# Optimization experiments

Measured on AMD Instinct MI355X. Metric: run time of the kernel, lower is better.

Reference implementation:

```python
import jax, jax.numpy as jnp
import numpy as np

N_NODES = 50000
N_EDGES = 800000
IN_DIM = 128
HID = 64
OUT_DIM = 128
N_GRAPHS = 256


def setup_inputs() -> dict:
    key = jax.random.key(0)
    ks = jax.random.split(key, 8)
    x = jax.random.normal(ks[0], (N_NODES, IN_DIM), dtype=jnp.float32)
    edge_index = jax.random.randint(ks[1], (2, N_EDGES), 0, N_NODES, dtype=jnp.int64)
    batch = jnp.sort(jax.random.randint(ks[2], (N_NODES,), 0, N_GRAPHS, dtype=jnp.int64))
    # Glorot-ish init for GCN weights, zero bias (PyG default bias=True)
    W1 = jax.random.normal(ks[3], (IN_DIM, HID), dtype=jnp.float32) / np.sqrt(IN_DIM)
    b1 = jnp.zeros((HID,), dtype=jnp.float32)
    W2 = jax.random.normal(ks[4], (HID, HID), dtype=jnp.float32) / np.sqrt(HID)
    b2 = jnp.zeros((HID,), dtype=jnp.float32)
    W3 = jax.random.normal(ks[5], (HID, OUT_DIM), dtype=jnp.float32) / np.sqrt(HID)
    b3 = jnp.zeros((OUT_DIM,), dtype=jnp.float32)
    return {"x": x, "edge_index": edge_index, "batch": batch, "num_graphs": N_GRAPHS,
            "W1": W1, "b1": b1, "W2": W2, "b2": b2, "W3": W3, "b3": b3}


def _gcn_norm(edge_index, n_nodes):
    # PyG GCNConv default: add self-loops, symmetric D^{-1/2}(A+I)D^{-1/2} norm.
    loops = jnp.arange(n_nodes, dtype=edge_index.dtype)
    src = jnp.concatenate([edge_index[0], loops])  # [E + N]
    dst = jnp.concatenate([edge_index[1], loops])
    deg = jax.ops.segment_sum(jnp.ones_like(dst, dtype=jnp.float32), dst,
                              num_segments=n_nodes)
    dinv = jnp.where(deg > 0, jax.lax.rsqrt(jnp.maximum(deg, 1.0)), 0.0)
    norm = dinv[src] * dinv[dst]  # [E + N]
    return src, dst, norm


def _gcn_conv(x, W, b, src, dst, norm, n_nodes):
    h = x @ W                                  # [N, F_out] dense GEMM
    msg = h[src] * norm[:, None]               # gather + scale  [E+N, F_out]
    agg = jax.ops.segment_sum(msg, dst, num_segments=n_nodes)
    return agg + b


def reference(x, edge_index, batch, num_graphs, W1, b1, W2, b2, W3, b3):
    n_nodes = x.shape[0]
    src, dst, norm = _gcn_norm(edge_index, n_nodes)
    h = jax.nn.gelu(_gcn_conv(x, W1, b1, src, dst, norm, n_nodes))
    h = jax.nn.gelu(_gcn_conv(h, W2, b2, src, dst, norm, n_nodes))
    h = _gcn_conv(h, W3, b3, src, dst, norm, n_nodes)
    # global_mean_pool over batch segment ids
    sums = jax.ops.segment_sum(h, batch, num_segments=num_graphs)
    counts = jax.ops.segment_sum(jnp.ones((n_nodes,), dtype=h.dtype), batch,
                                 num_segments=num_graphs)
    return sums / jnp.maximum(counts, 1.0)[:, None]
```

## Files before the change

### kernel.cpp

```cpp
#include <hip/hip_runtime.h>
#include <hip/hip_fp16.h>
#include <math.h>

#define N_NODES   50000
#define N_EDGES   800000
#define IN_DIM    128
#define HID       64
#define OUT_DIM   128
#define N_GRAPHS  256
#define MAX_DEG   64
#define PARTS     8
#define PSIZE     (N_NODES / PARTS)
#define EPB       4096
#define AGG_NPB   32

typedef _Float16 half8 __attribute__((ext_vector_type(8)));
typedef float floatx4 __attribute__((ext_vector_type(4)));


__global__ __launch_bounds__(256) void k_build(const int* __restrict__ src,
                                               const int* __restrict__ dst,
                                               int* __restrict__ deg, int* __restrict__ col) {
    int p     = blockIdx.x & (PARTS - 1);
    int chunk = blockIdx.x >> 3;
    int e0    = chunk * EPB + threadIdx.x * 16;
    if (e0 + 16 > N_EDGES) return;
    int lo = p * PSIZE, hi = lo + PSIZE;

    int dd[16], ss[16];
    const int4* d4 = (const int4*)(dst + e0);
    const int4* s4 = (const int4*)(src + e0);
#pragma unroll
    for (int j = 0; j < 4; j++) {
        int4 q = d4[j];
        dd[4 * j + 0] = q.x; dd[4 * j + 1] = q.y;
        dd[4 * j + 2] = q.z; dd[4 * j + 3] = q.w;
    }
#pragma unroll
    for (int j = 0; j < 4; j++) {
        int4 q = s4[j];
        ss[4 * j + 0] = q.x; ss[4 * j + 1] = q.y;
        ss[4 * j + 2] = q.z; ss[4 * j + 3] = q.w;
    }

    int pos[16];
#pragma unroll
    for (int j = 0; j < 16; j++) {
        pos[j] = -1;
        if (dd[j] >= lo && dd[j] < hi) pos[j] = atomicAdd(&deg[dd[j]], 1);
    }
#pragma unroll
    for (int j = 0; j < 16; j++) {
        if (pos[j] >= 0 && pos[j] < MAX_DEG)
            col[(size_t)dd[j] * MAX_DEG + pos[j]] = ss[j];
    }
}

__global__ __launch_bounds__(256) void k_prep(const int* __restrict__ deg,
                                              float* __restrict__ dinv,
                                              const float* __restrict__ W1, __half* __restrict__ Wt1,
                                              const float* __restrict__ W2, __half* __restrict__ Wt2) {
    int blk = blockIdx.x;
    if (blk < 196) {
        int n = blk * 256 + threadIdx.x;
        if (n < N_NODES) dinv[n] = rsqrtf((float)(deg[n] + 1));
    } else if (blk < 200) {
        int idx = (blk - 196) * 256 + threadIdx.x;
        int g = idx >> 6, n = idx & 63;
#pragma unroll
        for (int i = 0; i < 8; i++)
            Wt1[idx * 8 + i] = __float2half(W1[(8 * g + i) * 64 + n]);
    } else {
        int idx = (blk - 200) * 256 + threadIdx.x;
        if (idx < 512) {
            int g = idx >> 6, n = idx & 63;
#pragma unroll
            for (int i = 0; i < 8; i++)
                Wt2[idx * 8 + i] = __float2half(W2[(8 * g + i) * 64 + n]);
        }
    }
}


__global__ __launch_bounds__(256) void k_mfma1(const float* __restrict__ A,
                                               const float* __restrict__ dinv,
                                               const __half* __restrict__ Bp,
                                               __half* __restrict__ C) {
    constexpr int K = IN_DIM, S = K / 32;
    int wv   = threadIdx.x >> 6;
    int lane = threadIdx.x & 63;
    int quad = lane >> 4, l15 = lane & 15;
    int row0 = blockIdx.x * 64 + wv * 16;
    if (row0 >= N_NODES) return;

    half8 bf[S][4];
#pragma unroll
    for (int s = 0; s < S; s++)
#pragma unroll
        for (int j = 0; j < 4; j++)
            bf[s][j] = *(const half8*)(Bp + ((size_t)((4 * s + quad) * 64 + 16 * j + l15)) * 8);

    floatx4 acc[4];
#pragma unroll
    for (int j = 0; j < 4; j++) acc[j] = 0.f;

    int arow = row0 + l15;
    float dv = dinv[arow];
#pragma unroll
    for (int s = 0; s < S; s++) {
        float4 xa = *(const float4*)(A + (size_t)arow * K + 32 * s + quad * 8);
        float4 xb = *(const float4*)(A + (size_t)arow * K + 32 * s + quad * 8 + 4);
        half8 af;
        af[0] = (_Float16)(xa.x * dv); af[1] = (_Float16)(xa.y * dv);
        af[2] = (_Float16)(xa.z * dv); af[3] = (_Float16)(xa.w * dv);
        af[4] = (_Float16)(xb.x * dv); af[5] = (_Float16)(xb.y * dv);
        af[6] = (_Float16)(xb.z * dv); af[7] = (_Float16)(xb.w * dv);
#pragma unroll
        for (int j = 0; j < 4; j++)
            acc[j] = __builtin_amdgcn_mfma_f32_16x16x32_f16(af, bf[s][j], acc[j], 0, 0, 0);
    }
#pragma unroll
    for (int j = 0; j < 4; j++)
#pragma unroll
        for (int r = 0; r < 4; r++)
            C[(size_t)(row0 + quad * 4 + r) * 64 + 16 * j + l15] = __float2half(acc[j][r]);
}


__global__ __launch_bounds__(256) void k_mfma2(const __half* __restrict__ A,
                                               const __half* __restrict__ Bp,
                                               __half* __restrict__ C) {
    constexpr int K = HID, S = K / 32;
    int wv   = threadIdx.x >> 6;
    int lane = threadIdx.x & 63;
    int quad = lane >> 4, l15 = lane & 15;
    int row0 = blockIdx.x * 64 + wv * 16;
    if (row0 >= N_NODES) return;

    half8 bf[S][4];
#pragma unroll
    for (int s = 0; s < S; s++)
#pragma unroll
        for (int j = 0; j < 4; j++)
            bf[s][j] = *(const half8*)(Bp + ((size_t)((4 * s + quad) * 64 + 16 * j + l15)) * 8);

    floatx4 acc[4];
#pragma unroll
    for (int j = 0; j < 4; j++) acc[j] = 0.f;

    int arow = row0 + l15;
#pragma unroll
    for (int s = 0; s < S; s++) {
        half8 af = *(const half8*)(A + (size_t)arow * K + 32 * s + quad * 8);
#pragma unroll
        for (int j = 0; j < 4; j++)
            acc[j] = __builtin_amdgcn_mfma_f32_16x16x32_f16(af, bf[s][j], acc[j], 0, 0, 0);
    }
#pragma unroll
    for (int j = 0; j < 4; j++)
#pragma unroll
        for (int r = 0; r < 4; r++)
            C[(size_t)(row0 + quad * 4 + r) * 64 + 16 * j + l15] = __float2half(acc[j][r]);
}


__device__ __forceinline__ void add8(float* acc, uint4 v) {
    const __half2* h = (const __half2*)&v;
#pragma unroll
    for (int j = 0; j < 4; j++) {
        acc[2 * j]     += __low2float(h[j]);
        acc[2 * j + 1] += __high2float(h[j]);
    }
}

__global__ __launch_bounds__(256) void k_agg(const __half* __restrict__ T,
                                             const int* __restrict__ col,
                                             const int* __restrict__ indeg,
                                             const float* __restrict__ dinv,
                                             const float* __restrict__ b,
                                             __half* __restrict__ OUT, int mode) {
    __shared__ int cols[AGG_NPB][MAX_DEG + 1];
    __shared__ int sdeg[AGG_NPB];
    int base = blockIdx.x * AGG_NPB;

    if (threadIdx.x < AGG_NPB) {
        int g = base + threadIdx.x;
        int dg0 = (g < N_NODES) ? indeg[g] : 0;
        sdeg[threadIdx.x] = dg0 > MAX_DEG ? MAX_DEG : dg0;
    }
    __syncthreads();

    for (int idx = threadIdx.x; idx < AGG_NPB * MAX_DEG; idx += 256) {
        int r = idx >> 6, j = idx & 63;
        if (j < sdeg[r]) cols[r][j] = col[(size_t)(base + r) * MAX_DEG + j];
    }
    __syncthreads();

    int lane = threadIdx.x & 63;
    int wv   = threadIdx.x >> 6;
    int q = lane >> 3, t = lane & 7;
    int local = wv * 8 + q;
    int d = base + local;
    if (d >= N_NODES) return;

    int dg = sdeg[local];

    float acc[8];
#pragma unroll
    for (int j = 0; j < 8; j++) acc[j] = 0.f;
    add8(acc, *(const uint4*)(T + (size_t)d * HID + t * 8));

    const int* cl = cols[local];
    int i = 0;
    for (; i + 8 <= dg; i += 8) {
        uint4 v[8];
#pragma unroll
        for (int u = 0; u < 8; u++)
            v[u] = *(const uint4*)(T + (size_t)cl[i + u] * HID + t * 8);
#pragma unroll
        for (int u = 0; u < 8; u++) add8(acc, v[u]);
    }
    if (i + 4 <= dg) {
        uint4 v0 = *(const uint4*)(T + (size_t)cl[i] * HID + t * 8);
        uint4 v1 = *(const uint4*)(T + (size_t)cl[i + 1] * HID + t * 8);
        uint4 v2 = *(const uint4*)(T + (size_t)cl[i + 2] * HID + t * 8);
        uint4 v3 = *(const uint4*)(T + (size_t)cl[i + 3] * HID + t * 8);
        add8(acc, v0); add8(acc, v1); add8(acc, v2); add8(acc, v3);
        i += 4;
    }
    for (; i < dg; i++) {
        int s = cl[i];
        add8(acc, *(const uint4*)(T + (size_t)s * HID + t * 8));
    }

    float dv = dinv[d];
    float o[8];
#pragma unroll
    for (int j = 0; j < 8; j++) o[j] = acc[j] * dv;
    if (mode == 0) {
#pragma unroll
        for (int j = 0; j < 8; j++) {
            float v = o[j] + b[t * 8 + j];
            float u2 = 0.7978845608028654f * (v + 0.044715f * v * v * v);
            o[j] = 0.5f * v * (1.0f + tanhf(u2)) * dv;
        }
    }
    __half2 hh[4];
#pragma unroll
    for (int j = 0; j < 4; j++) hh[j] = __floats2half2_rn(o[2 * j], o[2 * j + 1]);
    *(uint4*)(OUT + (size_t)d * HID + t * 8) = *(uint4*)hh;
}


__global__ __launch_bounds__(256) void k_pool_out(const __half* __restrict__ A,
                                                  const int* __restrict__ batch,
                                                  const float* __restrict__ W3,
                                                  const float* __restrict__ b3,
                                                  float* __restrict__ out) {
    int g = blockIdx.x;
    int lo = 0, hi = N_NODES;
    while (lo < hi) { int m = (lo + hi) >> 1; if (batch[m] < g) lo = m + 1; else hi = m; }
    int lo2 = lo, hi2 = N_NODES;
    while (lo2 < hi2) { int m = (lo2 + hi2) >> 1; if (batch[m] < g + 1) lo2 = m + 1; else hi2 = m; }
    int start = lo, end = lo2;

    int lane = threadIdx.x & 63;
    int wave = threadIdx.x >> 6;
    float acc = 0.f;
    for (int n = start + wave; n < end; n += 4)
        acc += __half2float(A[(size_t)n * HID + lane]);

    __shared__ float part[4][HID];
    __shared__ float pooled[HID];
    part[wave][lane] = acc;
    __syncthreads();
    if (threadIdx.x < HID)
        pooled[threadIdx.x] = part[0][threadIdx.x] + part[1][threadIdx.x] +
                              part[2][threadIdx.x] + part[3][threadIdx.x];
    __syncthreads();

    if (threadIdx.x < OUT_DIM) {
        float cntf = (float)(end - start);
        float inv = 1.0f / fmaxf(cntf, 1.0f);
        float s = 0.f;
#pragma unroll
        for (int k = 0; k < HID; k++) s += pooled[k] * W3[k * OUT_DIM + threadIdx.x];
        out[g * OUT_DIM + threadIdx.x] = (s + cntf * b3[threadIdx.x]) * inv;
    }
}


extern "C" void kernel_launch(void* const* d_in, const int* in_sizes, int n_in,
                              void* d_out, int out_size, void* d_ws, size_t ws_size,
                              hipStream_t stream) {
    const float* x     = (const float*)d_in[0];
    const int*   ei    = (const int*)d_in[1];
    const int*   batch = (const int*)d_in[2];
    const float* W1    = (const float*)d_in[4];
    const float* b1    = (const float*)d_in[5];
    const float* W2    = (const float*)d_in[6];
    const float* b2    = (const float*)d_in[7];
    const float* W3    = (const float*)d_in[8];
    const float* b3    = (const float*)d_in[9];
    float* out = (float*)d_out;

    const int* esrc = ei;
    const int* edst = ei + N_EDGES;

    int*    deg  = (int*)d_ws;
    float*  dinv = (float*)(deg + N_NODES);
    int*    col  = (int*)(dinv + N_NODES);
    __half* t    = (__half*)(col + (size_t)N_NODES * MAX_DEG);
    __half* p    = t + (size_t)N_NODES * HID;
    __half* Wt1  = p + (size_t)N_NODES * HID;
    __half* Wt2  = Wt1 + IN_DIM * HID;

    hipMemsetAsync(deg, 0, (size_t)N_NODES * 4, stream);

    const int CHUNKS = (N_EDGES + EPB - 1) / EPB;
    k_build<<<CHUNKS * PARTS, 256, 0, stream>>>(esrc, edst, deg, col);
    k_prep<<<202, 256, 0, stream>>>(deg, dinv, W1, Wt1, W2, Wt2);

    const int GB = (N_NODES + 63) / 64;
    const int AB = (N_NODES + AGG_NPB - 1) / AGG_NPB;

    k_mfma1<<<GB, 256, 0, stream>>>(x, dinv, Wt1, t);
    k_agg<<<AB, 256, 0, stream>>>(t, col, deg, dinv, b1, p, 0);
    k_mfma2<<<GB, 256, 0, stream>>>(p, Wt2, t);
    k_agg<<<AB, 256, 0, stream>>>(t, col, deg, dinv, b2, p, 0);
    k_agg<<<AB, 256, 0, stream>>>(p, col, deg, dinv, b3, t, 1);
    k_pool_out<<<N_GRAPHS, 256, 0, stream>>>(t, batch, W3, b3, out);
}
```

Baseline: 233.6 us.

## Split 64-wide feature tensors into two 32-wide planes for cache-local gathers

Features are stored as two planar halves of 32 fp16 columns each, and each aggregation block handles one plane for 64 nodes. A gathered row segment is 64 bytes instead of 128, so the working set of each plane is half as large and fits better in L2 or the last-level cache during the random neighbour gathers. The column-list and output accesses also switch to nontemporal loads and stores. In exchange, every block reloads the column lists once per plane, doubling that index traffic, and the GEMM and pooling kernels now use strided plane addressing.

```diff
diff --git a/kernel.cpp b/kernel.cpp
--- a/kernel.cpp
+++ b/kernel.cpp
@@ -12,10 +12,12 @@
 #define PARTS     8
 #define PSIZE     (N_NODES / PARTS)
 #define EPB       4096
-#define AGG_NPB   32
+#define AGG_NPB   64
+#define PSTRIDE   ((size_t)N_NODES * 32)
 
 typedef _Float16 half8 __attribute__((ext_vector_type(8)));
 typedef float floatx4 __attribute__((ext_vector_type(4)));
+typedef unsigned int uintx4 __attribute__((ext_vector_type(4)));
 
 
 __global__ __launch_bounds__(256) void k_build(const int* __restrict__ src,
@@ -123,7 +125,8 @@
     for (int j = 0; j < 4; j++)
 #pragma unroll
         for (int r = 0; r < 4; r++)
-            C[(size_t)(row0 + quad * 4 + r) * 64 + 16 * j + l15] = __float2half(acc[j][r]);
+            C[(size_t)(j >> 1) * PSTRIDE + (size_t)(row0 + quad * 4 + r) * 32 +
+              16 * (j & 1) + l15] = __float2half(acc[j][r]);
 }
 
 
@@ -151,7 +154,7 @@
     int arow = row0 + l15;
 #pragma unroll
     for (int s = 0; s < S; s++) {
-        half8 af = *(const half8*)(A + (size_t)arow * K + 32 * s + quad * 8);
+        half8 af = *(const half8*)(A + (size_t)s * PSTRIDE + (size_t)arow * 32 + quad * 8);
 #pragma unroll
         for (int j = 0; j < 4; j++)
             acc[j] = __builtin_amdgcn_mfma_f32_16x16x32_f16(af, bf[s][j], acc[j], 0, 0, 0);
@@ -160,11 +163,12 @@
     for (int j = 0; j < 4; j++)
 #pragma unroll
         for (int r = 0; r < 4; r++)
-            C[(size_t)(row0 + quad * 4 + r) * 64 + 16 * j + l15] = __float2half(acc[j][r]);
-}
-
-
-__device__ __forceinline__ void add8(float* acc, uint4 v) {
+            C[(size_t)(j >> 1) * PSTRIDE + (size_t)(row0 + quad * 4 + r) * 32 +
+              16 * (j & 1) + l15] = __float2half(acc[j][r]);
+}
+
+
+__device__ __forceinline__ void add8(float* acc, uintx4 v) {
     const __half2* h = (const __half2*)&v;
 #pragma unroll
     for (int j = 0; j < 4; j++) {
@@ -181,7 +185,8 @@
                                              __half* __restrict__ OUT, int mode) {
     __shared__ int cols[AGG_NPB][MAX_DEG + 1];
     __shared__ int sdeg[AGG_NPB];
-    int base = blockIdx.x * AGG_NPB;
+    int plane = blockIdx.x & 1;
+    int base  = (blockIdx.x >> 1) * AGG_NPB;
 
     if (threadIdx.x < AGG_NPB) {
         int g = base + threadIdx.x;
@@ -192,46 +197,46 @@
 
     for (int idx = threadIdx.x; idx < AGG_NPB * MAX_DEG; idx += 256) {
         int r = idx >> 6, j = idx & 63;
-        if (j < sdeg[r]) cols[r][j] = col[(size_t)(base + r) * MAX_DEG + j];
+        if (j < sdeg[r])
+            cols[r][j] = __builtin_nontemporal_load(col + (size_t)(base + r) * MAX_DEG + j);
     }
     __syncthreads();
 
     int lane = threadIdx.x & 63;
     int wv   = threadIdx.x >> 6;
-    int q = lane >> 3, t = lane & 7;
-    int local = wv * 8 + q;
+    int q = lane >> 2, t = lane & 3;
+    int local = wv * 16 + q;
     int d = base + local;
     if (d >= N_NODES) return;
 
     int dg = sdeg[local];
+    const __half* P = T + (size_t)plane * PSTRIDE;
 
     float acc[8];
 #pragma unroll
     for (int j = 0; j < 8; j++) acc[j] = 0.f;
-    add8(acc, *(const uint4*)(T + (size_t)d * HID + t * 8));
+    add8(acc, *(const uintx4*)(P + (size_t)d * 32 + t * 8));
 
     const int* cl = cols[local];
     int i = 0;
     for (; i + 8 <= dg; i += 8) {
-        uint4 v[8];
+        uintx4 v[8];
 #pragma unroll
         for (int u = 0; u < 8; u++)
-            v[u] = *(const uint4*)(T + (size_t)cl[i + u] * HID + t * 8);
+            v[u] = *(const uintx4*)(P + (size_t)cl[i + u] * 32 + t * 8);
 #pragma unroll
         for (int u = 0; u < 8; u++) add8(acc, v[u]);
     }
     if (i + 4 <= dg) {
-        uint4 v0 = *(const uint4*)(T + (size_t)cl[i] * HID + t * 8);
-        uint4 v1 = *(const uint4*)(T + (size_t)cl[i + 1] * HID + t * 8);
-        uint4 v2 = *(const uint4*)(T + (size_t)cl[i + 2] * HID + t * 8);
-        uint4 v3 = *(const uint4*)(T + (size_t)cl[i + 3] * HID + t * 8);
+        uintx4 v0 = *(const uintx4*)(P + (size_t)cl[i] * 32 + t * 8);
+        uintx4 v1 = *(const uintx4*)(P + (size_t)cl[i + 1] * 32 + t * 8);
+        uintx4 v2 = *(const uintx4*)(P + (size_t)cl[i + 2] * 32 + t * 8);
+        uintx4 v3 = *(const uintx4*)(P + (size_t)cl[i + 3] * 32 + t * 8);
         add8(acc, v0); add8(acc, v1); add8(acc, v2); add8(acc, v3);
         i += 4;
     }
-    for (; i < dg; i++) {
-        int s = cl[i];
-        add8(acc, *(const uint4*)(T + (size_t)s * HID + t * 8));
-    }
+    for (; i < dg; i++)
+        add8(acc, *(const uintx4*)(P + (size_t)cl[i] * 32 + t * 8));
 
     float dv = dinv[d];
     float o[8];
@@ -240,7 +245,7 @@
     if (mode == 0) {
 #pragma unroll
         for (int j = 0; j < 8; j++) {
-            float v = o[j] + b[t * 8 + j];
+            float v = o[j] + b[plane * 32 + t * 8 + j];
             float u2 = 0.7978845608028654f * (v + 0.044715f * v * v * v);
             o[j] = 0.5f * v * (1.0f + tanhf(u2)) * dv;
         }
@@ -248,7 +253,11 @@
     __half2 hh[4];
 #pragma unroll
     for (int j = 0; j < 4; j++) hh[j] = __floats2half2_rn(o[2 * j], o[2 * j + 1]);
-    *(uint4*)(OUT + (size_t)d * HID + t * 8) = *(uint4*)hh;
+    uintx4 pack;
+#pragma unroll
+    for (int j = 0; j < 4; j++) pack[j] = *(unsigned int*)&hh[j];
+    __builtin_nontemporal_store(pack,
+        (uintx4*)(OUT + (size_t)plane * PSTRIDE + (size_t)d * 32 + t * 8));
 }
 
 
@@ -266,9 +275,10 @@
 
     int lane = threadIdx.x & 63;
     int wave = threadIdx.x >> 6;
+    const __half* Ap = A + (size_t)(lane >> 5) * PSTRIDE + (lane & 31);
     float acc = 0.f;
     for (int n = start + wave; n < end; n += 4)
-        acc += __half2float(A[(size_t)n * HID + lane]);
+        acc += __half2float(Ap[(size_t)n * 32]);
 
     __shared__ float part[4][HID];
     __shared__ float pooled[HID];
@@ -311,18 +321,18 @@
     float*  dinv = (float*)(deg + N_NODES);
     int*    col  = (int*)(dinv + N_NODES);
     __half* t    = (__half*)(col + (size_t)N_NODES * MAX_DEG);
-    __half* p    = t + (size_t)N_NODES * HID;
-    __half* Wt1  = p + (size_t)N_NODES * HID;
+    __half* p    = t + 2 * PSTRIDE;
+    __half* Wt1  = p + 2 * PSTRIDE;
     __half* Wt2  = Wt1 + IN_DIM * HID;
 
-    hipMemsetAsync(deg, 0, (size_t)N_NODES * 4, stream);
+    (void)hipMemsetAsync(deg, 0, (size_t)N_NODES * 4, stream);
 
     const int CHUNKS = (N_EDGES + EPB - 1) / EPB;
     k_build<<<CHUNKS * PARTS, 256, 0, stream>>>(esrc, edst, deg, col);
     k_prep<<<202, 256, 0, stream>>>(deg, dinv, W1, Wt1, W2, Wt2);
 
     const int GB = (N_NODES + 63) / 64;
-    const int AB = (N_NODES + AGG_NPB - 1) / AGG_NPB;
+    const int AB = 2 * ((N_NODES + AGG_NPB - 1) / AGG_NPB);
 
     k_mfma1<<<GB, 256, 0, stream>>>(x, dinv, Wt1, t);
     k_agg<<<AB, 256, 0, stream>>>(t, col, deg, dinv, b1, p, 0);
```

Measured after the change: 271.9 us. 16.4% more time.
